# Kernel optimization log

Hardware: AMD Instinct MI355X
Metric: run time of the kernel (lower is better)

The kernel has to match this reference:

```python
import jax, jax.numpy as jnp
import numpy as np

K = 16            # neighbors per node
NB = 8            # number_of_basis
MAX_RADIUS = 10.0
MUL_1E = 32       # multiplicity of the 1e output block
DIM_0E = 64       # 64x0e block (structurally zero: no 1o x 0e -> 0e path)
DIM_2E = 80       # 16x2e block (structurally zero: no 1o x 0e -> 2e path)


def knn_edges(coords):
    """coords [B,N,3] -> (senders, receivers) flat int32 indices of length B*N*K.
    Edge (j -> i): j is one of the K nearest neighbors of i (self excluded),
    matching torch_geometric knn_graph(loop=False, flow=source_to_target)."""
    B, N, _ = coords.shape
    n2 = jnp.sum(coords * coords, -1)                       # [B,N]
    d2 = n2[:, :, None] + n2[:, None, :] - 2.0 * jnp.einsum('bnd,bmd->bnm', coords, coords)
    d2 = d2 + jnp.eye(N, dtype=coords.dtype) * 1e10         # exclude self-loops
    _, idx = jax.lax.top_k(-d2, K)                          # [B,N,K] neighbor ids per node
    offs = (jnp.arange(B) * N)[:, None, None]
    senders = (idx + offs).reshape(-1)
    receivers = (jnp.broadcast_to(jnp.arange(N)[None, :, None], (B, N, K)) + offs).reshape(-1)
    return senders, receivers


def gaussian_soft_one_hot(x, number):
    # x in [0,1], shape [E,1] -> [E,number]
    centers = jnp.linspace(0.0, 1.0, number).astype(x.dtype)
    sigma = 1.0 / number
    g = jnp.exp(-(x - centers) ** 2 / (2.0 * sigma * sigma))
    s = jnp.sum(g, -1, keepdims=True)
    s = jnp.where(s > 0, s, jnp.ones_like(s))
    return g / s


def setup_inputs():
    key = jax.random.key(0)
    ks = jax.random.split(key, 6)
    B, N = 8, 4096
    coords = jax.random.normal(ks[0], (B, N, 3), dtype=jnp.float32) * 10.0
    atom_types = jax.random.randint(ks[1], (B, N), 0, 20)
    residue_types = jax.random.randint(ks[2], (B, N), 0, 21)
    tp_weight = jax.random.normal(ks[3], (NB, MUL_1E), dtype=jnp.float32) / np.sqrt(NB)
    atom_emb = jax.random.normal(ks[4], (20, 112), dtype=jnp.float32).at[0].set(0.0)   # padding_idx=0
    res_emb = jax.random.normal(ks[5], (21, 112), dtype=jnp.float32).at[0].set(0.0)    # padding_idx=0
    return {"coords": coords, "atom_types": atom_types, "residue_types": residue_types,
            "tp_weight": tp_weight, "atom_emb": atom_emb, "res_emb": res_emb}


def reference(coords, atom_types, residue_types, tp_weight, atom_emb, res_emb):
    B, N, _ = coords.shape
    E = B * N * K
    senders, receivers = knn_edges(coords)
    cf = coords.reshape(-1, 3)
    r = cf[senders] - cf[receivers]                           # [E,3]
    dist = jnp.linalg.norm(r, axis=-1, keepdims=True)         # [E,1]
    r_hat = r / (dist + 1e-8)
    cutoff = jnp.clip(dist / MAX_RADIUS, 0.0, 1.0)
    rb = gaussian_soft_one_hot(cutoff, NB)                    # [E,NB]
    # FullyConnectedTensorProduct(1x1o/1e, NBx0e -> ... 32x1e ...):
    feat_1e = jnp.einsum('ev,vw,em->ewm', rb, tp_weight, r_hat) / np.sqrt(3.0)  # [E,32,3]
    # scatter_mean over receivers
    num = jax.ops.segment_sum(feat_1e.reshape(E, MUL_1E * 3), receivers, num_segments=B * N)
    cnt = jax.ops.segment_sum(jnp.ones((E,), coords.dtype), receivers, num_segments=B * N)
    agg_1e = (num / jnp.maximum(cnt, 1.0)[:, None]).reshape(B, N, MUL_1E * 3)
    zeros0 = jnp.zeros((B, N, DIM_0E), coords.dtype)
    zeros2 = jnp.zeros((B, N, DIM_2E), coords.dtype)
    pos_feats = jnp.concatenate([zeros0, agg_1e, zeros2], -1)  # [B,N,240]
    node_features = jnp.concatenate([pos_feats, atom_emb[atom_types], res_emb[residue_types]], -1)
    return node_features  # [B,N,464]
```

## Files before the change

### kernel.cpp

```cpp
#include <hip/hip_runtime.h>
#include <hip/hip_bf16.h>

#define NN    4096
#define KNEI  16
#define QPW   4
#define WPB   16
#define BLOCK (WPB * 64)
#define QPB   (WPB * QPW)
#define NEGB  -3.0e38f
#define PACKM 0xFFFFFFC0

typedef float f32x2 __attribute__((ext_vector_type(2)));
typedef int   i32x2 __attribute__((ext_vector_type(2)));

__device__ __forceinline__ int rlane(int v, int l)
{ return __builtin_amdgcn_readlane(v, l); }
__device__ __forceinline__ float rlanef(float v, int l)
{ return __int_as_float(__builtin_amdgcn_readlane(__float_as_int(v), l)); }

template<int CTRL>
__device__ __forceinline__ float rmax_step(float f)
{
    int s_ = __builtin_amdgcn_update_dpp(__float_as_int(f), __float_as_int(f),
                                         CTRL, 0xF, 0xF, false);
    return fmaxf(f, __int_as_float(s_));
}

template<int CTRL>
__device__ __forceinline__ void amax_step(float& f, int& i)
{
    int fs = __builtin_amdgcn_update_dpp(__float_as_int(f), __float_as_int(f),
                                         CTRL, 0xF, 0xF, false);
    int is = __builtin_amdgcn_update_dpp(i, i, CTRL, 0xF, 0xF, false);
    float ff = __int_as_float(fs);
    bool gt = ff > f;
    f = gt ? ff : f;
    i = gt ? is : i;
}

__device__ __forceinline__ void wave_amax(float f, int i, float& M, int& mi)
{
    amax_step<0x111>(f, i); amax_step<0x112>(f, i); amax_step<0x114>(f, i);
    amax_step<0x118>(f, i); amax_step<0x142>(f, i); amax_step<0x143>(f, i);
    M  = rlanef(f, 63);
    mi = rlane(i, 63);
}

__device__ __forceinline__ float row16_sum_dpp(float v)
{
    float f = v;
#define STEPA(CTRL)                                                          \
    { int s_ = __builtin_amdgcn_update_dpp(0, __float_as_int(f),             \
               (CTRL), 0xF, 0xF, true);                                      \
      f += __int_as_float(s_); }
    STEPA(0x111) STEPA(0x112) STEPA(0x114) STEPA(0x118)
#undef STEPA
    return f;
}

__device__ __forceinline__ float bpermf(int abyte, float v)
{ return __int_as_float(__builtin_amdgcn_ds_bpermute(abyte, __float_as_int(v))); }

__device__ __forceinline__ float sel4f(float a, float b, float c, float d, int q)
{
    float lo = (q & 1) ? b : a;
    float hi = (q & 1) ? d : c;
    return (q & 2) ? hi : lo;
}

#define SELFFIX(q, b, s)                                                     \
    {  int cb_ = __float_as_int(b) & 63;                                     \
       if ((((cb_) << 6) | (lane ^ cb_)) == q0 + (q)) { (b) = (s); (s) = NEGB; } \
       int cs_ = __float_as_int(s) & 63;                                     \
       if ((((cs_) << 6) | (lane ^ cs_)) == q0 + (q)) { (s) = NEGB; } }

#define REPLAY(qq, xq, yq, zq)                                               \
    {   int wq = __ffsll(ex & (0xFFFFull << ((qq) * 16))) - 1;               \
        int colq = rlane(col, wq);                                           \
        int kq   = rlane(kf,  wq);                                           \
        int j2 = (lane << 6) | (colq ^ lane);                                \
        float4 Pp = pts[j2];                                                 \
        float scr = fmaf(Pp.x,(xq), fmaf(Pp.y,(yq), fmaf(Pp.z,(zq), Pp.w))); \
        float sf = __int_as_float((__float_as_int(scr) & PACKM) | lane);     \
        if (j2 == q0 + (qq)) sf = NEGB;                                      \
        const int4* sp = (const int4*)&sel[wv * 64 + ((qq) << 4)];           \
        int4 sa = sp[0], sb = sp[1], sc = sp[2], sd = sp[3];                 \
        if (j2==sa.x || j2==sa.y || j2==sa.z || j2==sa.w) sf = NEGB;         \
        if (j2==sb.x || j2==sb.y || j2==sb.z || j2==sb.w) sf = NEGB;         \
        if (j2==sc.x || j2==sc.y || j2==sc.z || j2==sc.w) sf = NEGB;         \
        if (j2==sd.x || j2==sd.y || j2==sd.z || j2==sd.w) sf = NEGB;         \
        float M1; int i1;                                                    \
        wave_amax(sf, j2, M1, i1);                                           \
        float sf2 = (j2 == i1) ? NEGB : sf;                                  \
        float M2; int i2;                                                    \
        wave_amax(sf2, j2, M2, i2);                                          \
        bool ow = (lane == (qq) * 16 + (colq & 15));                         \
        if (kq == 0)      { pb0 = ow ? M1 : pb0; ps0 = ow ? M2 : ps0; }      \
        else if (kq == 1) { pb1 = ow ? M1 : pb1; ps1 = ow ? M2 : ps1; }      \
        else if (kq == 2) { pb2 = ow ? M1 : pb2; ps2 = ow ? M2 : ps2; }      \
        else              { pb3 = ow ? M1 : pb3; ps3 = ow ? M2 : ps3; }      \
    }

__global__ __launch_bounds__(BLOCK, 8)
void protein_enc_kernel(const float* __restrict__ coords,
                        const int*   __restrict__ atypes,
                        const int*   __restrict__ rtypes,
                        const float* __restrict__ tpw,
                        const float* __restrict__ aemb,
                        const float* __restrict__ remb,
                        float* __restrict__ out)
{
    __shared__ float4 pts[NN];
    __shared__ float  sW[8 * 32];
    __shared__ int    sel[WPB * 64];

    const int tid  = threadIdx.x;
    const int lane = tid & 63;
    const int wv   = tid >> 6;
    const int bpb  = NN / QPB;
    const int batch    = blockIdx.x / bpb;
    const int nodeBase = (blockIdx.x % bpb) * QPB;

    const float* cb = coords + (size_t)batch * NN * 3;

    for (int p = tid; p < NN; p += BLOCK) {
        float x = cb[3*p], y = cb[3*p+1], z = cb[3*p+2];
        pts[p] = make_float4(x, y, z, -0.5f * (x*x + y*y + z*z));
    }
    if (tid < 256) sW[tid] = tpw[tid];
    sel[wv * 64 + lane] = -1;
    __syncthreads();

    const int q0 = nodeBase + wv * QPW;
    const float4 P0 = pts[q0],   P1 = pts[q0+1];
    const float4 P2 = pts[q0+2], P3 = pts[q0+3];
    const float x0 = P0.x, y0 = P0.y, z0 = P0.z;
    const float x1 = P1.x, y1 = P1.y, z1 = P1.z;
    const float x2 = P2.x, y2 = P2.y, z2 = P2.z;
    const float x3 = P3.x, y3 = P3.y, z3 = P3.z;

    const f32x2 qAx = {x0, x1}, qAy = {y0, y1}, qAz = {z0, z1};
    const f32x2 qBx = {x2, x3}, qBy = {y2, y3}, qBz = {z2, z3};
    const i32x2 M2v = {(int)PACKM, (int)PACKM};

    f32x2 bA = {NEGB, NEGB}, sA = {NEGB, NEGB};
    f32x2 bB = {NEGB, NEGB}, sB = {NEGB, NEGB};

    #pragma unroll 8
    for (int c = 0; c < NN / 64; ++c) {
        int j = (c << 6) | (lane ^ c);
        float4 P = pts[j];
        f32x2 vx = {P.x, P.x}, vy = {P.y, P.y}, vz = {P.z, P.z}, vw = {P.w, P.w};
        f32x2 dA = __builtin_elementwise_fma(vx, qAx,
                   __builtin_elementwise_fma(vy, qAy,
                   __builtin_elementwise_fma(vz, qAz, vw)));
        f32x2 dB = __builtin_elementwise_fma(vx, qBx,
                   __builtin_elementwise_fma(vy, qBy,
                   __builtin_elementwise_fma(vz, qBz, vw)));
        i32x2 cc = {c, c};
        f32x2 pA = __builtin_bit_cast(f32x2,
                     (__builtin_bit_cast(i32x2, dA) & M2v) | cc);
        f32x2 pB = __builtin_bit_cast(f32x2,
                     (__builtin_bit_cast(i32x2, dB) & M2v) | cc);
        sA = __builtin_elementwise_max(sA, __builtin_elementwise_min(pA, bA));
        bA = __builtin_elementwise_max(bA, pA);
        sB = __builtin_elementwise_max(sB, __builtin_elementwise_min(pB, bB));
        bB = __builtin_elementwise_max(bB, pB);
    }

    float b0 = bA.x, b1 = bA.y, b2 = bB.x, b3 = bB.y;
    float s0 = sA.x, s1 = sA.y, s2 = sB.x, s3 = sB.y;

    SELFFIX(0, b0, s0)
    SELFFIX(1, b1, s1)
    SELFFIX(2, b2, s2)
    SELFFIX(3, b3, s3)

    const int q  = lane >> 4;
    const int gt = lane & 15;
    float pb0, pb1, pb2, pb3, ps0, ps1, ps2, ps3;
    {
        const int ab = gt << 2;
#define PULL(K, PB, PS)                                                      \
        {   int a = ab + ((K) << 6);                                         \
            PB = sel4f(bpermf(a,b0), bpermf(a,b1), bpermf(a,b2), bpermf(a,b3), q); \
            PS = sel4f(bpermf(a,s0), bpermf(a,s1), bpermf(a,s2), bpermf(a,s3), q); \
        }
        PULL(0, pb0, ps0)
        PULL(1, pb1, ps1)
        PULL(2, pb2, ps2)
        PULL(3, pb3, ps3)
#undef PULL
    }

    const unsigned long long gmask = 0xFFFFull << (q << 4);
    const int selbase = wv * 64 + (q << 4);

    #pragma unroll 1
    for (int r = 0; r < KNEI; ++r) {
        float f = fmaxf(fmaxf(pb0, pb1), fmaxf(pb2, pb3));
        f = rmax_step<0x121>(f); f = rmax_step<0x122>(f);
        f = rmax_step<0x124>(f); f = rmax_step<0x128>(f);
        bool c0 = (pb0 == f), c1 = (pb1 == f), c2 = (pb2 == f), c3 = (pb3 == f);
        unsigned long long m = __ballot(c0 | c1 | c2 | c3);
        int w = __ffsll(m & gmask) - 1;
        bool iwin = (lane == w);
        int kf = c0 ? 0 : (c1 ? 1 : (c2 ? 2 : 3));
        bool o0 = iwin && c0;
        bool o1 = iwin && !c0 && c1;
        bool o2 = iwin && !c0 && !c1 && c2;
        bool o3 = iwin && !c0 && !c1 && !c2;
        int cw  = __float_as_int(f) & 63;
        int col = gt + (kf << 4);
        int jw  = (cw << 6) | (col ^ cw);
        if (iwin) sel[selbase + r] = jw;
        float pskf = o1 ? ps1 : (o2 ? ps2 : (o3 ? ps3 : ps0));
        bool e = iwin && (pskf == NEGB);
        pb0 = o0 ? ps0 : pb0;  ps0 = o0 ? NEGB : ps0;
        pb1 = o1 ? ps1 : pb1;  ps1 = o1 ? NEGB : ps1;
        pb2 = o2 ? ps2 : pb2;  ps2 = o2 ? NEGB : ps2;
        pb3 = o3 ? ps3 : pb3;  ps3 = o3 ? NEGB : ps3;
        unsigned long long ex = __ballot(e);
        if (ex) {
            if ((ex >>  0) & 0xFFFFull) REPLAY(0, x0, y0, z0)
            if ((ex >> 16) & 0xFFFFull) REPLAY(1, x1, y1, z1)
            if ((ex >> 32) & 0xFFFFull) REPLAY(2, x2, y2, z2)
            if ((ex >> 48) & 0xFFFFull) REPLAY(3, x3, y3, z3)
        }
    }

    int selIdx = sel[wv * 64 + lane];

    float xq = (q & 2) ? ((q & 1) ? x3 : x2) : ((q & 1) ? x1 : x0);
    float yq = (q & 2) ? ((q & 1) ? y3 : y2) : ((q & 1) ? y1 : y0);
    float zq = (q & 2) ? ((q & 1) ? z3 : z2) : ((q & 1) ? z1 : z0);

    float4 P = pts[selIdx];
    float rx = P.x - xq, ry = P.y - yq, rz = P.z - zq;
    float dist = sqrtf(rx*rx + ry*ry + rz*rz);
    float inv  = 1.0f / (dist + 1e-8f);
    float hx = rx * inv, hy = ry * inv, hz = rz * inv;
    float cu = fminf(dist / 10.0f, 1.0f);
    float A = expf(cu * cu * -32.0f);
    float E = expf(cu * (64.0f / 7.0f));
    const float K[8] = {1.0f, 0.5204501f, 0.0733697f, 0.00280164f,
                        2.897772e-05f, 8.11857e-08f, 6.16130e-11f,
                        1.2664166e-14f};
    float gg[8];
    float t = A, ssum = A;
    gg[0] = A;
    #pragma unroll
    for (int v = 1; v < 8; ++v) { t *= E; gg[v] = t * K[v]; ssum += gg[v]; }
    float is = 1.0f / ssum;
    float S[24];
    #pragma unroll
    for (int v = 0; v < 8; ++v) {
        float rbv = gg[v] * is;
        S[3*v]   = rbv * hx;
        S[3*v+1] = rbv * hy;
        S[3*v+2] = rbv * hz;
    }
    #pragma unroll
    for (int t2 = 0; t2 < 24; ++t2) S[t2] = row16_sum_dpp(S[t2]);

    float wcol[8];
    #pragma unroll
    for (int v = 0; v < 8; ++v) wcol[v] = sW[32*v + (lane & 31)];

    const float scale = 0.036084391824351613f;
    const float4 z4 = make_float4(0.f, 0.f, 0.f, 0.f);

    #pragma unroll
    for (int qq = 0; qq < QPW; ++qq) {
        const int gq = batch * NN + q0 + qq;
        float sg[24];
        #pragma unroll
        for (int t2 = 0; t2 < 24; ++t2) sg[t2] = rlanef(S[t2], 16 * qq + 15);

        float* onode = out + (size_t)gq * 464;
        float4* o4 = (float4*)onode;
        if (lane < 16)       o4[lane] = z4;
        else if (lane < 36)  o4[lane + 24] = z4;

        if (lane < 32) {
            float a0 = 0.f, a1 = 0.f, a2 = 0.f;
            #pragma unroll
            for (int v = 0; v < 8; ++v) {
                a0 = fmaf(wcol[v], sg[3*v],   a0);
                a1 = fmaf(wcol[v], sg[3*v+1], a1);
                a2 = fmaf(wcol[v], sg[3*v+2], a2);
            }
            onode[64 + 3*lane]     = a0 * scale;
            onode[64 + 3*lane + 1] = a1 * scale;
            onode[64 + 3*lane + 2] = a2 * scale;
        }

        const int at = atypes[gq];
        const int rt = rtypes[gq];
        if (lane < 56) {
            float4 v = (lane < 28)
                ? ((const float4*)(aemb + 112*at))[lane]
                : ((const float4*)(remb + 112*rt))[lane - 28];
            o4[60 + lane] = v;
        }
    }
}

extern "C" void kernel_launch(void* const* d_in, const int* in_sizes, int n_in,
                              void* d_out, int out_size, void* d_ws, size_t ws_size,
                              hipStream_t stream)
{
    const float* coords = (const float*)d_in[0];
    const int*   at     = (const int*)  d_in[1];
    const int*   rt     = (const int*)  d_in[2];
    const float* tpw    = (const float*)d_in[3];
    const float* ae     = (const float*)d_in[4];
    const float* re     = (const float*)d_in[5];
    float* out = (float*)d_out;

    const int B = in_sizes[1] / NN;
    dim3 grid(B * (NN / QPB));
    protein_enc_kernel<<<grid, BLOCK, 0, stream>>>(coords, at, rt, tpw, ae, re, out);
}
```

Before: 73.71 us.

## Process eight queries per wave with dual interleaved top-k selection streams

```diff
diff --git a/kernel.cpp b/kernel.cpp
--- a/kernel.cpp
+++ b/kernel.cpp
@@ -3,7 +3,7 @@
 
 #define NN    4096
 #define KNEI  16
-#define QPW   4
+#define QPW   8
 #define WPB   16
 #define BLOCK (WPB * 64)
 #define QPB   (WPB * QPW)
@@ -24,6 +24,21 @@
     int s_ = __builtin_amdgcn_update_dpp(__float_as_int(f), __float_as_int(f),
                                          CTRL, 0xF, 0xF, false);
     return fmaxf(f, __int_as_float(s_));
+}
+
+template<int CTRL>
+__device__ __forceinline__ float radd_step(float f)
+{
+    int s_ = __builtin_amdgcn_update_dpp(__float_as_int(f), __float_as_int(f),
+                                         CTRL, 0xF, 0xF, false);
+    return f + __int_as_float(s_);
+}
+
+__device__ __forceinline__ float row16_allsum(float v)
+{
+    v = radd_step<0x121>(v); v = radd_step<0x122>(v);
+    v = radd_step<0x124>(v); v = radd_step<0x128>(v);
+    return v;
 }
 
 template<int CTRL>
@@ -46,18 +61,6 @@
     mi = rlane(i, 63);
 }
 
-__device__ __forceinline__ float row16_sum_dpp(float v)
-{
-    float f = v;
-#define STEPA(CTRL)                                                          \
-    { int s_ = __builtin_amdgcn_update_dpp(0, __float_as_int(f),             \
-               (CTRL), 0xF, 0xF, true);                                      \
-      f += __int_as_float(s_); }
-    STEPA(0x111) STEPA(0x112) STEPA(0x114) STEPA(0x118)
-#undef STEPA
-    return f;
-}
-
 __device__ __forceinline__ float bpermf(int abyte, float v)
 { return __int_as_float(__builtin_amdgcn_ds_bpermute(abyte, __float_as_int(v))); }
 
@@ -74,168 +77,45 @@
        int cs_ = __float_as_int(s) & 63;                                     \
        if ((((cs_) << 6) | (lane ^ cs_)) == q0 + (q)) { (s) = NEGB; } }
 
-#define REPLAY(qq, xq, yq, zq)                                               \
-    {   int wq = __ffsll(ex & (0xFFFFull << ((qq) * 16))) - 1;               \
-        int colq = rlane(col, wq);                                           \
-        int kq   = rlane(kf,  wq);                                           \
-        int j2 = (lane << 6) | (colq ^ lane);                                \
-        float4 Pp = pts[j2];                                                 \
-        float scr = fmaf(Pp.x,(xq), fmaf(Pp.y,(yq), fmaf(Pp.z,(zq), Pp.w))); \
-        float sf = __int_as_float((__float_as_int(scr) & PACKM) | lane);     \
-        if (j2 == q0 + (qq)) sf = NEGB;                                      \
-        const int4* sp = (const int4*)&sel[wv * 64 + ((qq) << 4)];           \
-        int4 sa = sp[0], sb = sp[1], sc = sp[2], sd = sp[3];                 \
-        if (j2==sa.x || j2==sa.y || j2==sa.z || j2==sa.w) sf = NEGB;         \
-        if (j2==sb.x || j2==sb.y || j2==sb.z || j2==sb.w) sf = NEGB;         \
-        if (j2==sc.x || j2==sc.y || j2==sc.z || j2==sc.w) sf = NEGB;         \
-        if (j2==sd.x || j2==sd.y || j2==sd.z || j2==sd.w) sf = NEGB;         \
-        float M1; int i1;                                                    \
-        wave_amax(sf, j2, M1, i1);                                           \
-        float sf2 = (j2 == i1) ? NEGB : sf;                                  \
-        float M2; int i2;                                                    \
-        wave_amax(sf2, j2, M2, i2);                                          \
-        bool ow = (lane == (qq) * 16 + (colq & 15));                         \
-        if (kq == 0)      { pb0 = ow ? M1 : pb0; ps0 = ow ? M2 : ps0; }      \
-        else if (kq == 1) { pb1 = ow ? M1 : pb1; ps1 = ow ? M2 : ps1; }      \
-        else if (kq == 2) { pb2 = ow ? M1 : pb2; ps2 = ow ? M2 : ps2; }      \
-        else              { pb3 = ow ? M1 : pb3; ps3 = ow ? M2 : ps3; }      \
-    }
-
-__global__ __launch_bounds__(BLOCK, 8)
-void protein_enc_kernel(const float* __restrict__ coords,
-                        const int*   __restrict__ atypes,
-                        const int*   __restrict__ rtypes,
-                        const float* __restrict__ tpw,
-                        const float* __restrict__ aemb,
-                        const float* __restrict__ remb,
-                        float* __restrict__ out)
-{
-    __shared__ float4 pts[NN];
-    __shared__ float  sW[8 * 32];
-    __shared__ int    sel[WPB * 64];
-
-    const int tid  = threadIdx.x;
-    const int lane = tid & 63;
-    const int wv   = tid >> 6;
-    const int bpb  = NN / QPB;
-    const int batch    = blockIdx.x / bpb;
-    const int nodeBase = (blockIdx.x % bpb) * QPB;
-
-    const float* cb = coords + (size_t)batch * NN * 3;
-
-    for (int p = tid; p < NN; p += BLOCK) {
-        float x = cb[3*p], y = cb[3*p+1], z = cb[3*p+2];
-        pts[p] = make_float4(x, y, z, -0.5f * (x*x + y*y + z*z));
-    }
-    if (tid < 256) sW[tid] = tpw[tid];
-    sel[wv * 64 + lane] = -1;
-    __syncthreads();
-
-    const int q0 = nodeBase + wv * QPW;
-    const float4 P0 = pts[q0],   P1 = pts[q0+1];
-    const float4 P2 = pts[q0+2], P3 = pts[q0+3];
-    const float x0 = P0.x, y0 = P0.y, z0 = P0.z;
-    const float x1 = P1.x, y1 = P1.y, z1 = P1.z;
-    const float x2 = P2.x, y2 = P2.y, z2 = P2.z;
-    const float x3 = P3.x, y3 = P3.y, z3 = P3.z;
-
-    const f32x2 qAx = {x0, x1}, qAy = {y0, y1}, qAz = {z0, z1};
-    const f32x2 qBx = {x2, x3}, qBy = {y2, y3}, qBz = {z2, z3};
-    const i32x2 M2v = {(int)PACKM, (int)PACKM};
-
-    f32x2 bA = {NEGB, NEGB}, sA = {NEGB, NEGB};
-    f32x2 bB = {NEGB, NEGB}, sB = {NEGB, NEGB};
-
-    #pragma unroll 8
-    for (int c = 0; c < NN / 64; ++c) {
-        int j = (c << 6) | (lane ^ c);
-        float4 P = pts[j];
-        f32x2 vx = {P.x, P.x}, vy = {P.y, P.y}, vz = {P.z, P.z}, vw = {P.w, P.w};
-        f32x2 dA = __builtin_elementwise_fma(vx, qAx,
-                   __builtin_elementwise_fma(vy, qAy,
-                   __builtin_elementwise_fma(vz, qAz, vw)));
-        f32x2 dB = __builtin_elementwise_fma(vx, qBx,
-                   __builtin_elementwise_fma(vy, qBy,
-                   __builtin_elementwise_fma(vz, qBz, vw)));
-        i32x2 cc = {c, c};
-        f32x2 pA = __builtin_bit_cast(f32x2,
-                     (__builtin_bit_cast(i32x2, dA) & M2v) | cc);
-        f32x2 pB = __builtin_bit_cast(f32x2,
-                     (__builtin_bit_cast(i32x2, dB) & M2v) | cc);
-        sA = __builtin_elementwise_max(sA, __builtin_elementwise_min(pA, bA));
-        bA = __builtin_elementwise_max(bA, pA);
-        sB = __builtin_elementwise_max(sB, __builtin_elementwise_min(pB, bB));
-        bB = __builtin_elementwise_max(bB, pB);
-    }
-
-    float b0 = bA.x, b1 = bA.y, b2 = bB.x, b3 = bB.y;
-    float s0 = sA.x, s1 = sA.y, s2 = sB.x, s3 = sB.y;
-
-    SELFFIX(0, b0, s0)
-    SELFFIX(1, b1, s1)
-    SELFFIX(2, b2, s2)
-    SELFFIX(3, b3, s3)
-
-    const int q  = lane >> 4;
-    const int gt = lane & 15;
-    float pb0, pb1, pb2, pb3, ps0, ps1, ps2, ps3;
-    {
-        const int ab = gt << 2;
-#define PULL(K, PB, PS)                                                      \
-        {   int a = ab + ((K) << 6);                                         \
-            PB = sel4f(bpermf(a,b0), bpermf(a,b1), bpermf(a,b2), bpermf(a,b3), q); \
-            PS = sel4f(bpermf(a,s0), bpermf(a,s1), bpermf(a,s2), bpermf(a,s3), q); \
-        }
-        PULL(0, pb0, ps0)
-        PULL(1, pb1, ps1)
-        PULL(2, pb2, ps2)
-        PULL(3, pb3, ps3)
-#undef PULL
-    }
-
-    const unsigned long long gmask = 0xFFFFull << (q << 4);
-    const int selbase = wv * 64 + (q << 4);
-
-    #pragma unroll 1
-    for (int r = 0; r < KNEI; ++r) {
-        float f = fmaxf(fmaxf(pb0, pb1), fmaxf(pb2, pb3));
-        f = rmax_step<0x121>(f); f = rmax_step<0x122>(f);
-        f = rmax_step<0x124>(f); f = rmax_step<0x128>(f);
-        bool c0 = (pb0 == f), c1 = (pb1 == f), c2 = (pb2 == f), c3 = (pb3 == f);
-        unsigned long long m = __ballot(c0 | c1 | c2 | c3);
-        int w = __ffsll(m & gmask) - 1;
-        bool iwin = (lane == w);
-        int kf = c0 ? 0 : (c1 ? 1 : (c2 ? 2 : 3));
-        bool o0 = iwin && c0;
-        bool o1 = iwin && !c0 && c1;
-        bool o2 = iwin && !c0 && !c1 && c2;
-        bool o3 = iwin && !c0 && !c1 && !c2;
-        int cw  = __float_as_int(f) & 63;
-        int col = gt + (kf << 4);
-        int jw  = (cw << 6) | (col ^ cw);
-        if (iwin) sel[selbase + r] = jw;
-        float pskf = o1 ? ps1 : (o2 ? ps2 : (o3 ? ps3 : ps0));
-        bool e = iwin && (pskf == NEGB);
-        pb0 = o0 ? ps0 : pb0;  ps0 = o0 ? NEGB : ps0;
-        pb1 = o1 ? ps1 : pb1;  ps1 = o1 ? NEGB : ps1;
-        pb2 = o2 ? ps2 : pb2;  ps2 = o2 ? NEGB : ps2;
-        pb3 = o3 ? ps3 : pb3;  ps3 = o3 ? NEGB : ps3;
-        unsigned long long ex = __ballot(e);
-        if (ex) {
-            if ((ex >>  0) & 0xFFFFull) REPLAY(0, x0, y0, z0)
-            if ((ex >> 16) & 0xFFFFull) REPLAY(1, x1, y1, z1)
-            if ((ex >> 32) & 0xFFFFull) REPLAY(2, x2, y2, z2)
-            if ((ex >> 48) & 0xFFFFull) REPLAY(3, x3, y3, z3)
-        }
-    }
-
-    int selIdx = sel[wv * 64 + lane];
-
-    float xq = (q & 2) ? ((q & 1) ? x3 : x2) : ((q & 1) ? x1 : x0);
-    float yq = (q & 2) ? ((q & 1) ? y3 : y2) : ((q & 1) ? y1 : y0);
-    float zq = (q & 2) ? ((q & 1) ? z3 : z2) : ((q & 1) ? z1 : z0);
-
-    float4 P = pts[selIdx];
+__device__ __forceinline__ void replay_q(const float4* __restrict__ pts,
+    const int* __restrict__ selp, int qLoc, float xq, float yq, float zq,
+    unsigned long long exq, int colv, int kfv, int lane, int ownerBase,
+    float& pb0, float& pb1, float& pb2, float& pb3,
+    float& ps0, float& ps1, float& ps2, float& ps3)
+{
+    int wq = __ffsll((unsigned long long)exq) - 1;
+    int colq = rlane(colv, wq);
+    int kq   = rlane(kfv,  wq);
+    int j2 = (lane << 6) | (colq ^ lane);
+    float4 Pp = pts[j2];
+    float scr = fmaf(Pp.x, xq, fmaf(Pp.y, yq, fmaf(Pp.z, zq, Pp.w)));
+    float sf = __int_as_float((__float_as_int(scr) & PACKM) | lane);
+    if (j2 == qLoc) sf = NEGB;
+    const int4* sp = (const int4*)selp;
+    int4 sa = sp[0], sb = sp[1], sc = sp[2], sd = sp[3];
+    if (j2==sa.x || j2==sa.y || j2==sa.z || j2==sa.w) sf = NEGB;
+    if (j2==sb.x || j2==sb.y || j2==sb.z || j2==sb.w) sf = NEGB;
+    if (j2==sc.x || j2==sc.y || j2==sc.z || j2==sc.w) sf = NEGB;
+    if (j2==sd.x || j2==sd.y || j2==sd.z || j2==sd.w) sf = NEGB;
+    float M1; int i1;
+    wave_amax(sf, j2, M1, i1);
+    float sf2 = (j2 == i1) ? NEGB : sf;
+    float M2; int i2;
+    wave_amax(sf2, j2, M2, i2);
+    bool ow = (lane == ownerBase + (colq & 15));
+    if (kq == 0)      { pb0 = ow ? M1 : pb0; ps0 = ow ? M2 : ps0; }
+    else if (kq == 1) { pb1 = ow ? M1 : pb1; ps1 = ow ? M2 : ps1; }
+    else if (kq == 2) { pb2 = ow ? M1 : pb2; ps2 = ow ? M2 : ps2; }
+    else              { pb3 = ow ? M1 : pb3; ps3 = ow ? M2 : ps3; }
+}
+
+__device__ __forceinline__ void emit_query(const float4* __restrict__ pts,
+    const float* __restrict__ sW, const int* __restrict__ atypes,
+    const int* __restrict__ rtypes, const float* __restrict__ aemb,
+    const float* __restrict__ remb, float* __restrict__ out,
+    int gq, int esel, float xq, float yq, float zq, int gt)
+{
+    float4 P = pts[esel];
     float rx = P.x - xq, ry = P.y - yq, rz = P.z - zq;
     float dist = sqrtf(rx*rx + ry*ry + rz*rz);
     float inv  = 1.0f / (dist + 1e-8f);
@@ -261,49 +141,263 @@
         S[3*v+2] = rbv * hz;
     }
     #pragma unroll
-    for (int t2 = 0; t2 < 24; ++t2) S[t2] = row16_sum_dpp(S[t2]);
-
-    float wcol[8];
+    for (int t2 = 0; t2 < 24; ++t2) S[t2] = row16_allsum(S[t2]);
+
+    float* onode = out + (size_t)gq * 464;
+    float4* o4 = (float4*)onode;
+    const float4 z4 = make_float4(0.f, 0.f, 0.f, 0.f);
+    o4[gt] = z4;
+    o4[40 + gt] = z4;
+    if (gt < 4) o4[56 + gt] = z4;
+
+    const float scale = 0.036084391824351613f;
+    float a0 = 0.f, a1 = 0.f, a2 = 0.f;
+    float c0 = 0.f, c1 = 0.f, c2 = 0.f;
     #pragma unroll
-    for (int v = 0; v < 8; ++v) wcol[v] = sW[32*v + (lane & 31)];
-
-    const float scale = 0.036084391824351613f;
-    const float4 z4 = make_float4(0.f, 0.f, 0.f, 0.f);
-
+    for (int v = 0; v < 8; ++v) {
+        float w0 = sW[32*v + gt];
+        float w1 = sW[32*v + gt + 16];
+        a0 = fmaf(w0, S[3*v],   a0);
+        a1 = fmaf(w0, S[3*v+1], a1);
+        a2 = fmaf(w0, S[3*v+2], a2);
+        c0 = fmaf(w1, S[3*v],   c0);
+        c1 = fmaf(w1, S[3*v+1], c1);
+        c2 = fmaf(w1, S[3*v+2], c2);
+    }
+    onode[64 + 3*gt]          = a0 * scale;
+    onode[64 + 3*gt + 1]      = a1 * scale;
+    onode[64 + 3*gt + 2]      = a2 * scale;
+    onode[64 + 3*(gt+16)]     = c0 * scale;
+    onode[64 + 3*(gt+16) + 1] = c1 * scale;
+    onode[64 + 3*(gt+16) + 2] = c2 * scale;
+
+    const int at = atypes[gq];
+    const int rt = rtypes[gq];
     #pragma unroll
-    for (int qq = 0; qq < QPW; ++qq) {
-        const int gq = batch * NN + q0 + qq;
-        float sg[24];
-        #pragma unroll
-        for (int t2 = 0; t2 < 24; ++t2) sg[t2] = rlanef(S[t2], 16 * qq + 15);
-
-        float* onode = out + (size_t)gq * 464;
-        float4* o4 = (float4*)onode;
-        if (lane < 16)       o4[lane] = z4;
-        else if (lane < 36)  o4[lane + 24] = z4;
-
-        if (lane < 32) {
-            float a0 = 0.f, a1 = 0.f, a2 = 0.f;
-            #pragma unroll
-            for (int v = 0; v < 8; ++v) {
-                a0 = fmaf(wcol[v], sg[3*v],   a0);
-                a1 = fmaf(wcol[v], sg[3*v+1], a1);
-                a2 = fmaf(wcol[v], sg[3*v+2], a2);
-            }
-            onode[64 + 3*lane]     = a0 * scale;
-            onode[64 + 3*lane + 1] = a1 * scale;
-            onode[64 + 3*lane + 2] = a2 * scale;
+    for (int rr = 0; rr < 4; ++rr) {
+        int idx = gt + 16*rr;
+        if (idx < 56) {
+            float4 v = (idx < 28)
+                ? ((const float4*)(aemb + 112*at))[idx]
+                : ((const float4*)(remb + 112*rt))[idx - 28];
+            o4[60 + idx] = v;
         }
-
-        const int at = atypes[gq];
-        const int rt = rtypes[gq];
-        if (lane < 56) {
-            float4 v = (lane < 28)
-                ? ((const float4*)(aemb + 112*at))[lane]
-                : ((const float4*)(remb + 112*rt))[lane - 28];
-            o4[60 + lane] = v;
+    }
+}
+
+__global__ __launch_bounds__(BLOCK, 4)
+void protein_enc_kernel(const float* __restrict__ coords,
+                        const int*   __restrict__ atypes,
+                        const int*   __restrict__ rtypes,
+                        const float* __restrict__ tpw,
+                        const float* __restrict__ aemb,
+                        const float* __restrict__ remb,
+                        float* __restrict__ out)
+{
+    __shared__ float4 pts[NN];
+    __shared__ float  sW[8 * 32];
+    __shared__ int    sel[WPB * 128];
+
+    const int tid  = threadIdx.x;
+    const int lane = tid & 63;
+    const int wv   = tid >> 6;
+    const int bpb  = NN / QPB;
+    const int batch    = blockIdx.x / bpb;
+    const int nodeBase = (blockIdx.x % bpb) * QPB;
+
+    const float* cb = coords + (size_t)batch * NN * 3;
+
+    for (int p = tid; p < NN; p += BLOCK) {
+        float x = cb[3*p], y = cb[3*p+1], z = cb[3*p+2];
+        pts[p] = make_float4(x, y, z, -0.5f * (x*x + y*y + z*z));
+    }
+    if (tid < 256) sW[tid] = tpw[tid];
+    sel[wv*128 + lane] = -1;
+    sel[wv*128 + 64 + lane] = -1;
+    __syncthreads();
+
+    const int q0 = nodeBase + wv * QPW;
+    const float4 Pq0 = pts[q0+0], Pq1 = pts[q0+1], Pq2 = pts[q0+2], Pq3 = pts[q0+3];
+    const float4 Pq4 = pts[q0+4], Pq5 = pts[q0+5], Pq6 = pts[q0+6], Pq7 = pts[q0+7];
+    const float x0=Pq0.x, y0=Pq0.y, z0=Pq0.z, x1=Pq1.x, y1=Pq1.y, z1=Pq1.z;
+    const float x2=Pq2.x, y2=Pq2.y, z2=Pq2.z, x3=Pq3.x, y3=Pq3.y, z3=Pq3.z;
+    const float x4=Pq4.x, y4=Pq4.y, z4v=Pq4.z, x5=Pq5.x, y5=Pq5.y, z5=Pq5.z;
+    const float x6=Pq6.x, y6=Pq6.y, z6=Pq6.z, x7=Pq7.x, y7=Pq7.y, z7=Pq7.z;
+
+    const f32x2 qx01={x0,x1}, qy01={y0,y1}, qz01={z0,z1};
+    const f32x2 qx23={x2,x3}, qy23={y2,y3}, qz23={z2,z3};
+    const f32x2 qx45={x4,x5}, qy45={y4,y5}, qz45={z4v,z5};
+    const f32x2 qx67={x6,x7}, qy67={y6,y7}, qz67={z6,z7};
+    const i32x2 MKv = {(int)PACKM, (int)PACKM};
+
+    f32x2 b01={NEGB,NEGB}, s01={NEGB,NEGB}, b23={NEGB,NEGB}, s23={NEGB,NEGB};
+    f32x2 b45={NEGB,NEGB}, s45={NEGB,NEGB}, b67={NEGB,NEGB}, s67={NEGB,NEGB};
+
+    #pragma unroll 8
+    for (int c = 0; c < NN / 64; ++c) {
+        int j = (c << 6) | (lane ^ c);
+        float4 P = pts[j];
+        f32x2 vx = {P.x, P.x}, vy = {P.y, P.y}, vz = {P.z, P.z}, vw = {P.w, P.w};
+        f32x2 d01 = __builtin_elementwise_fma(vx, qx01,
+                    __builtin_elementwise_fma(vy, qy01,
+                    __builtin_elementwise_fma(vz, qz01, vw)));
+        f32x2 d23 = __builtin_elementwise_fma(vx, qx23,
+                    __builtin_elementwise_fma(vy, qy23,
+                    __builtin_elementwise_fma(vz, qz23, vw)));
+        f32x2 d45 = __builtin_elementwise_fma(vx, qx45,
+                    __builtin_elementwise_fma(vy, qy45,
+                    __builtin_elementwise_fma(vz, qz45, vw)));
+        f32x2 d67 = __builtin_elementwise_fma(vx, qx67,
+                    __builtin_elementwise_fma(vy, qy67,
+                    __builtin_elementwise_fma(vz, qz67, vw)));
+        i32x2 cc = {c, c};
+        f32x2 p01 = __builtin_bit_cast(f32x2,(__builtin_bit_cast(i32x2,d01)&MKv)|cc);
+        f32x2 p23 = __builtin_bit_cast(f32x2,(__builtin_bit_cast(i32x2,d23)&MKv)|cc);
+        f32x2 p45 = __builtin_bit_cast(f32x2,(__builtin_bit_cast(i32x2,d45)&MKv)|cc);
+        f32x2 p67 = __builtin_bit_cast(f32x2,(__builtin_bit_cast(i32x2,d67)&MKv)|cc);
+        s01 = __builtin_elementwise_max(s01, __builtin_elementwise_min(p01, b01));
+        b01 = __builtin_elementwise_max(b01, p01);
+        s23 = __builtin_elementwise_max(s23, __builtin_elementwise_min(p23, b23));
+        b23 = __builtin_elementwise_max(b23, p23);
+        s45 = __builtin_elementwise_max(s45, __builtin_elementwise_min(p45, b45));
+        b45 = __builtin_elementwise_max(b45, p45);
+        s67 = __builtin_elementwise_max(s67, __builtin_elementwise_min(p67, b67));
+        b67 = __builtin_elementwise_max(b67, p67);
+    }
+
+    float bb0=b01.x, bb1=b01.y, bb2=b23.x, bb3=b23.y;
+    float bb4=b45.x, bb5=b45.y, bb6=b67.x, bb7=b67.y;
+    float ss0=s01.x, ss1=s01.y, ss2=s23.x, ss3=s23.y;
+    float ss4=s45.x, ss5=s45.y, ss6=s67.x, ss7=s67.y;
+
+    SELFFIX(0, bb0, ss0) SELFFIX(1, bb1, ss1) SELFFIX(2, bb2, ss2)
+    SELFFIX(3, bb3, ss3) SELFFIX(4, bb4, ss4) SELFFIX(5, bb5, ss5)
+    SELFFIX(6, bb6, ss6) SELFFIX(7, bb7, ss7)
+
+    const int g  = lane >> 4;
+    const int gt = lane & 15;
+    float pbA0,pbA1,pbA2,pbA3, psA0,psA1,psA2,psA3;
+    float pbB0,pbB1,pbB2,pbB3, psB0,psB1,psB2,psB3;
+#define PULL(K, PBA, PBB, PSA, PSB)                                          \
+    {   int a = (gt + ((K) << 4)) << 2;                                      \
+        float t0=bpermf(a,bb0), t1=bpermf(a,bb1), t2=bpermf(a,bb2),          \
+              t3=bpermf(a,bb3), t4=bpermf(a,bb4), t5=bpermf(a,bb5),          \
+              t6=bpermf(a,bb6), t7=bpermf(a,bb7);                            \
+        PBA = sel4f(t0, t2, t4, t6, g);                                      \
+        PBB = sel4f(t1, t3, t5, t7, g);                                      \
+        float u0=bpermf(a,ss0), u1=bpermf(a,ss1), u2=bpermf(a,ss2),          \
+              u3=bpermf(a,ss3), u4=bpermf(a,ss4), u5=bpermf(a,ss5),          \
+              u6=bpermf(a,ss6), u7=bpermf(a,ss7);                            \
+        PSA = sel4f(u0, u2, u4, u6, g);                                      \
+        PSB = sel4f(u1, u3, u5, u7, g);                                      \
+    }
+    PULL(0, pbA0, pbB0, psA0, psB0)
+    PULL(1, pbA1, pbB1, psA1, psB1)
+    PULL(2, pbA2, pbB2, psA2, psB2)
+    PULL(3, pbA3, pbB3, psA3, psB3)
+#undef PULL
+
+    const unsigned long long gmask = 0xFFFFull << (g << 4);
+    int* selpA = &sel[wv*128 + (g << 5)];
+    int* selpB = selpA + 16;
+
+    #pragma unroll 1
+    for (int r = 0; r < KNEI; ++r) {
+        float fA = fmaxf(fmaxf(pbA0, pbA1), fmaxf(pbA2, pbA3));
+        float fB = fmaxf(fmaxf(pbB0, pbB1), fmaxf(pbB2, pbB3));
+        fA = rmax_step<0x121>(fA); fB = rmax_step<0x121>(fB);
+        fA = rmax_step<0x122>(fA); fB = rmax_step<0x122>(fB);
+        fA = rmax_step<0x124>(fA); fB = rmax_step<0x124>(fB);
+        fA = rmax_step<0x128>(fA); fB = rmax_step<0x128>(fB);
+        bool cA0=(pbA0==fA), cA1=(pbA1==fA), cA2=(pbA2==fA), cA3=(pbA3==fA);
+        bool cB0=(pbB0==fB), cB1=(pbB1==fB), cB2=(pbB2==fB), cB3=(pbB3==fB);
+        unsigned long long mA = __ballot(cA0|cA1|cA2|cA3);
+        unsigned long long mB = __ballot(cB0|cB1|cB2|cB3);
+        int wA = __ffsll(mA & gmask) - 1;
+        int wB = __ffsll(mB & gmask) - 1;
+        bool iwinA = (lane == wA), iwinB = (lane == wB);
+        int kfA = cA0 ? 0 : (cA1 ? 1 : (cA2 ? 2 : 3));
+        int kfB = cB0 ? 0 : (cB1 ? 1 : (cB2 ? 2 : 3));
+        int cwA = __float_as_int(fA) & 63;
+        int cwB = __float_as_int(fB) & 63;
+        int colA = gt + (kfA << 4), colB = gt + (kfB << 4);
+        int jA = (cwA << 6) | (colA ^ cwA);
+        int jB = (cwB << 6) | (colB ^ cwB);
+        if (iwinA) selpA[r] = jA;
+        if (iwinB) selpB[r] = jB;
+        bool oA0 = iwinA && cA0;
+        bool oA1 = iwinA && !cA0 && cA1;
+        bool oA2 = iwinA && !cA0 && !cA1 && cA2;
+        bool oA3 = iwinA && !cA0 && !cA1 && !cA2;
+        bool oB0 = iwinB && cB0;
+        bool oB1 = iwinB && !cB0 && cB1;
+        bool oB2 = iwinB && !cB0 && !cB1 && cB2;
+        bool oB3 = iwinB && !cB0 && !cB1 && !cB2;
+        float pskA = oA1 ? psA1 : (oA2 ? psA2 : (oA3 ? psA3 : psA0));
+        float pskB = oB1 ? psB1 : (oB2 ? psB2 : (oB3 ? psB3 : psB0));
+        bool eA = iwinA && (pskA == NEGB);
+        bool eB = iwinB && (pskB == NEGB);
+        pbA0 = oA0 ? psA0 : pbA0;  psA0 = oA0 ? NEGB : psA0;
+        pbA1 = oA1 ? psA1 : pbA1;  psA1 = oA1 ? NEGB : psA1;
+        pbA2 = oA2 ? psA2 : pbA2;  psA2 = oA2 ? NEGB : psA2;
+        pbA3 = oA3 ? psA3 : pbA3;  psA3 = oA3 ? NEGB : psA3;
+        pbB0 = oB0 ? psB0 : pbB0;  psB0 = oB0 ? NEGB : psB0;
+        pbB1 = oB1 ? psB1 : pbB1;  psB1 = oB1 ? NEGB : psB1;
+        pbB2 = oB2 ? psB2 : pbB2;  psB2 = oB2 ? NEGB : psB2;
+        pbB3 = oB3 ? psB3 : pbB3;  psB3 = oB3 ? NEGB : psB3;
+        unsigned long long exA = __ballot(eA);
+        unsigned long long exB = __ballot(eB);
+        if (exA | exB) {
+            if (exA & 0x000000000000FFFFull)
+                replay_q(pts, &sel[wv*128+  0], q0+0, x0,y0,z0,
+                         exA & 0x000000000000FFFFull, colA, kfA, lane, 0,
+                         pbA0,pbA1,pbA2,pbA3, psA0,psA1,psA2,psA3);
+            if (exB & 0x000000000000FFFFull)
+                replay_q(pts, &sel[wv*128+ 16], q0+1, x1,y1,z1,
+                         exB & 0x000000000000FFFFull, colB, kfB, lane, 0,
+                         pbB0,pbB1,pbB2,pbB3, psB0,psB1,psB2,psB3);
+            if (exA & 0x00000000FFFF0000ull)
+                replay_q(pts, &sel[wv*128+ 32], q0+2, x2,y2,z2,
+                         exA & 0x00000000FFFF0000ull, colA, kfA, lane, 16,
+                         pbA0,pbA1,pbA2,pbA3, psA0,psA1,psA2,psA3);
+            if (exB & 0x00000000FFFF0000ull)
+                replay_q(pts, &sel[wv*128+ 48], q0+3, x3,y3,z3,
+                         exB & 0x00000000FFFF0000ull, colB, kfB, lane, 16,
+                         pbB0,pbB1,pbB2,pbB3, psB0,psB1,psB2,psB3);
+            if (exA & 0x0000FFFF00000000ull)
+                replay_q(pts, &sel[wv*128+ 64], q0+4, x4,y4,z4v,
+                         exA & 0x0000FFFF00000000ull, colA, kfA, lane, 32,
+                         pbA0,pbA1,pbA2,pbA3, psA0,psA1,psA2,psA3);
+            if (exB & 0x0000FFFF00000000ull)
+                replay_q(pts, &sel[wv*128+ 80], q0+5, x5,y5,z5,
+                         exB & 0x0000FFFF00000000ull, colB, kfB, lane, 32,
+                         pbB0,pbB1,pbB2,pbB3, psB0,psB1,psB2,psB3);
+            if (exA & 0xFFFF000000000000ull)
+                replay_q(pts, &sel[wv*128+ 96], q0+6, x6,y6,z6,
+                         exA & 0xFFFF000000000000ull, colA, kfA, lane, 48,
+                         pbA0,pbA1,pbA2,pbA3, psA0,psA1,psA2,psA3);
+            if (exB & 0xFFFF000000000000ull)
+                replay_q(pts, &sel[wv*128+112], q0+7, x7,y7,z7,
+                         exB & 0xFFFF000000000000ull, colB, kfB, lane, 48,
+                         pbB0,pbB1,pbB2,pbB3, psB0,psB1,psB2,psB3);
         }
     }
+
+    float xqA = sel4f(x0, x2, x4, x6, g);
+    float yqA = sel4f(y0, y2, y4, y6, g);
+    float zqA = sel4f(z0, z2, z4v, z6, g);
+    float xqB = sel4f(x1, x3, x5, x7, g);
+    float yqB = sel4f(y1, y3, y5, y7, g);
+    float zqB = sel4f(z1, z3, z5, z7, g);
+
+    int eselA = selpA[gt];
+    int eselB = selpB[gt];
+    int gqA = batch * NN + q0 + 2*g;
+
+    emit_query(pts, sW, atypes, rtypes, aemb, remb, out,
+               gqA,     eselA, xqA, yqA, zqA, gt);
+    emit_query(pts, sW, atypes, rtypes, aemb, remb, out,
+               gqA + 1, eselB, xqB, yqB, zqB, gt);
 }
 
 extern "C" void kernel_launch(void* const* d_in, const int* in_sizes, int n_in,
```

Result: slower. 86.98 us (+18.0%).

## Software-pipeline LDS point loads with double-buffered register batches in kNN scan

Applied to the files above, without the earlier changes.

```diff
diff --git a/kernel.cpp b/kernel.cpp
--- a/kernel.cpp
+++ b/kernel.cpp
@@ -101,7 +101,38 @@
         else              { pb3 = ow ? M1 : pb3; ps3 = ow ? M2 : ps3; }      \
     }
 
-__global__ __launch_bounds__(BLOCK, 8)
+#define LOAD8(BUF, CG)                                                       \
+    _Pragma("unroll")                                                        \
+    for (int u = 0; u < 8; ++u) {                                            \
+        int c_ = (CG) * 8 + u;                                               \
+        BUF[u] = pts[(c_ << 6) | (lane ^ c_)];                               \
+    }
+
+#define COMP8(BUF, CG)                                                       \
+    _Pragma("unroll")                                                        \
+    for (int u = 0; u < 8; ++u) {                                            \
+        int c_ = (CG) * 8 + u;                                               \
+        float4 P = BUF[u];                                                   \
+        f32x2 vx = {P.x, P.x}, vy = {P.y, P.y};                              \
+        f32x2 vz = {P.z, P.z}, vw = {P.w, P.w};                              \
+        f32x2 dA = __builtin_elementwise_fma(vx, qAx,                        \
+                   __builtin_elementwise_fma(vy, qAy,                        \
+                   __builtin_elementwise_fma(vz, qAz, vw)));                 \
+        f32x2 dB = __builtin_elementwise_fma(vx, qBx,                        \
+                   __builtin_elementwise_fma(vy, qBy,                        \
+                   __builtin_elementwise_fma(vz, qBz, vw)));                 \
+        i32x2 cc = {c_, c_};                                                 \
+        f32x2 pA = __builtin_bit_cast(f32x2,                                 \
+                     (__builtin_bit_cast(i32x2, dA) & M2v) | cc);            \
+        f32x2 pB = __builtin_bit_cast(f32x2,                                 \
+                     (__builtin_bit_cast(i32x2, dB) & M2v) | cc);            \
+        sA = __builtin_elementwise_max(sA, __builtin_elementwise_min(pA, bA)); \
+        bA = __builtin_elementwise_max(bA, pA);                              \
+        sB = __builtin_elementwise_max(sB, __builtin_elementwise_min(pB, bB)); \
+        bB = __builtin_elementwise_max(bB, pB);                              \
+    }
+
+__global__ __launch_bounds__(BLOCK, 4)
 void protein_enc_kernel(const float* __restrict__ coords,
                         const int*   __restrict__ atypes,
                         const int*   __restrict__ rtypes,
@@ -146,26 +177,19 @@
     f32x2 bA = {NEGB, NEGB}, sA = {NEGB, NEGB};
     f32x2 bB = {NEGB, NEGB}, sB = {NEGB, NEGB};
 
-    #pragma unroll 8
-    for (int c = 0; c < NN / 64; ++c) {
-        int j = (c << 6) | (lane ^ c);
-        float4 P = pts[j];
-        f32x2 vx = {P.x, P.x}, vy = {P.y, P.y}, vz = {P.z, P.z}, vw = {P.w, P.w};
-        f32x2 dA = __builtin_elementwise_fma(vx, qAx,
-                   __builtin_elementwise_fma(vy, qAy,
-                   __builtin_elementwise_fma(vz, qAz, vw)));
-        f32x2 dB = __builtin_elementwise_fma(vx, qBx,
-                   __builtin_elementwise_fma(vy, qBy,
-                   __builtin_elementwise_fma(vz, qBz, vw)));
-        i32x2 cc = {c, c};
-        f32x2 pA = __builtin_bit_cast(f32x2,
-                     (__builtin_bit_cast(i32x2, dA) & M2v) | cc);
-        f32x2 pB = __builtin_bit_cast(f32x2,
-                     (__builtin_bit_cast(i32x2, dB) & M2v) | cc);
-        sA = __builtin_elementwise_max(sA, __builtin_elementwise_min(pA, bA));
-        bA = __builtin_elementwise_max(bA, pA);
-        sB = __builtin_elementwise_max(sB, __builtin_elementwise_min(pB, bB));
-        bB = __builtin_elementwise_max(bB, pB);
+    {
+        float4 Pa[8], Pb[8];
+        LOAD8(Pa, 0)
+        #pragma unroll 1
+        for (int cg = 0; cg < 6; cg += 2) {
+            LOAD8(Pb, cg + 1)
+            COMP8(Pa, cg)
+            LOAD8(Pa, cg + 2)
+            COMP8(Pb, cg + 1)
+        }
+        LOAD8(Pb, 7)
+        COMP8(Pa, 6)
+        COMP8(Pb, 7)
     }
 
     float b0 = bA.x, b1 = bA.y, b2 = bB.x, b3 = bB.y;
```

Result: slower. 82.68 us (+12.2%).
